# Performance work log

Measured on AMD Instinct MI355X. Metric: run time of the kernel, lower is better.

Reference implementation:

```python
import jax, jax.numpy as jnp
import numpy as np

EMB = 1024
NHEAD = 16
HEAD_DIM = EMB // NHEAD  # 64
L = 2048
NEG = -1e30


def setup_inputs() -> dict:
    key = jax.random.key(0)
    ks = jax.random.split(key, 8)
    # xavier_uniform bound for square [EMB, EMB] matrices
    bound = float(np.sqrt(6.0 / (EMB + EMB)))
    def xavier(k):
        return jax.random.uniform(k, (EMB, EMB), jnp.float32, -bound, bound)
    return {
        "q": jax.random.normal(ks[0], (L, EMB), jnp.float32),
        "k": jax.random.normal(ks[1], (L, EMB), jnp.float32),
        "v": jax.random.normal(ks[2], (L, EMB), jnp.float32),
        "mask": jax.random.randint(ks[3], (NHEAD, L, L), 0, 2) > 0,
        "Wq": xavier(ks[4]),
        "Wk": xavier(ks[5]),
        "Wv": xavier(ks[6]),
        "Wo": xavier(ks[7]),
    }


def reference(q, k, v, mask, Wq, Wk, Wv, Wo):
    scaling = HEAD_DIM ** -0.5
    # F.linear(x, W) = x @ W.T ; reshape to [H, L, D]
    Q = (q @ Wq.T).reshape(L, NHEAD, HEAD_DIM).swapaxes(0, 1)
    K = (k @ Wk.T).reshape(L, NHEAD, HEAD_DIM).swapaxes(0, 1)
    V = (v @ Wv.T).reshape(L, NHEAD, HEAD_DIM).swapaxes(0, 1)
    scores = jnp.einsum("hld,hmd->hlm", Q, K) * scaling  # [H, L, L]
    scores = jnp.where(mask, jnp.asarray(NEG, scores.dtype), scores)
    p = jax.nn.softmax(scores, axis=-1)
    # attn_mask=True: multiplicative re-mask after softmax (custom path)
    p = p * (~mask).astype(p.dtype)
    # dropout is a no-op in eval mode
    attn_out = jnp.einsum("hlm,hmd->hld", p, V)  # [H, L, D]
    attn_out = attn_out.swapaxes(0, 1).reshape(L, EMB)
    return attn_out @ Wo.T
```

## Files before the change

### kernel.cpp

```cpp
#include <hip/hip_runtime.h>
#include <stdint.h>

#define EMB   1024
#define NHEAD 16
#define HDIM  64
#define SEQ   2048

typedef unsigned short ushort_t;
typedef unsigned int   uint32;
typedef __attribute__((ext_vector_type(8))) short bfrag;
typedef __attribute__((ext_vector_type(4))) float ffrag;

#define MFMA(a, b, c) __builtin_amdgcn_mfma_f32_16x16x32_bf16((a), (b), (c), 0, 0, 0)

__device__ inline ushort_t f2bf(float f) {
  uint32 u = __float_as_uint(f);
  u += 0x7FFFu + ((u >> 16) & 1u);
  return (ushort_t)(u >> 16);
}
__device__ inline uint32 pack2(float a, float b) {
  return (uint32)f2bf(a) | ((uint32)f2bf(b) << 16);
}

__device__ inline void glds16(const ushort_t* g, ushort_t* l) {
  __builtin_amdgcn_global_load_lds(
      (const __attribute__((address_space(1))) uint32*)(uintptr_t)g,
      (__attribute__((address_space(3))) uint32*)(uintptr_t)l, 16, 0, 0);
}

__global__ void detect_mask_kernel(const uint32* __restrict__ mw, int* __restrict__ flag) {
  uint32 w = mw[threadIdx.x];
  bool is4 = (w == 0u) || (w == 1u) || (w == 0x3F800000u);
  unsigned long long bad = __ballot(!is4);
  if (threadIdx.x == 0) flag[0] = (bad == 0ull) ? 1 : 0;
}

__global__ __launch_bounds__(256) void compress_mask(
    const void* __restrict__ maskp, const int* __restrict__ flag, ushort_t* __restrict__ bm)
{
  size_t t = (size_t)blockIdx.x * 256 + threadIdx.x;
  size_t row = t >> 7;
  int c16 = (int)(t & 127);
  size_t base = row * SEQ + (size_t)c16 * 16;
  ushort_t mv = 0;
  if (*flag) {
    const uint4* p = (const uint4*)((const uint32*)maskp + base);
    uint4 a0 = p[0], a1 = p[1], a2 = p[2], a3 = p[3];
    uint32 aw[16] = {a0.x,a0.y,a0.z,a0.w, a1.x,a1.y,a1.z,a1.w,
                     a2.x,a2.y,a2.z,a2.w, a3.x,a3.y,a3.z,a3.w};
    #pragma unroll
    for (int i = 0; i < 16; ++i) mv |= (ushort_t)((aw[i] != 0u) ? 1u : 0u) << i;
  } else {
    uint4 b0 = *(const uint4*)((const unsigned char*)maskp + base);
    uint32 bw[4] = {b0.x, b0.y, b0.z, b0.w};
    #pragma unroll
    for (int i = 0; i < 16; ++i)
      mv |= (ushort_t)((((bw[i >> 2] >> ((i & 3) * 8)) & 0xFFu) != 0u) ? 1u : 0u) << i;
  }
  bm[t] = mv;
}

__global__ __launch_bounds__(256) void cvt_all(
    const float4* __restrict__ q,  const float4* __restrict__ k,  const float4* __restrict__ v,
    const float4* __restrict__ wq, const float4* __restrict__ wk, const float4* __restrict__ wv,
    const float4* __restrict__ wo,
    uint2* __restrict__ qb,  uint2* __restrict__ kb,  uint2* __restrict__ vb,
    uint2* __restrict__ wqb, uint2* __restrict__ wkb, uint2* __restrict__ wvb,
    uint2* __restrict__ wob)
{
  int t = blockIdx.x * 256 + threadIdx.x;
  int s = blockIdx.y;
  const float4* src; uint2* dst; int n4;
  switch (s) {
    case 0: src = q;  dst = qb;  n4 = (SEQ * EMB) / 4; break;
    case 1: src = k;  dst = kb;  n4 = (SEQ * EMB) / 4; break;
    case 2: src = v;  dst = vb;  n4 = (SEQ * EMB) / 4; break;
    case 3: src = wq; dst = wqb; n4 = (EMB * EMB) / 4; break;
    case 4: src = wk; dst = wkb; n4 = (EMB * EMB) / 4; break;
    case 5: src = wv; dst = wvb; n4 = (EMB * EMB) / 4; break;
    default: src = wo; dst = wob; n4 = (EMB * EMB) / 4; break;
  }
  if (t >= n4) return;
  float4 f = src[t];
  uint2 o; o.x = pack2(f.x, f.y); o.y = pack2(f.z, f.w);
  dst[t] = o;
}

template<int MODE, int BN>
__device__ inline void gemm_body(const ushort_t* A, const ushort_t* B, void* Cp,
                                 int m0, int n0, ushort_t* As, ushort_t* Bs) {
  const int tid = threadIdx.x, lane = tid & 63, w = tid >> 6;
  const int wm = (w >> 1) * 64, wn = (w & 1) * (BN / 2);
  const int col = lane & 15, g = lane >> 4;
  constexpr int TN = BN / 32;
  constexpr int BIT = BN / 32;

  ffrag acc[4][TN] = {};

  for (int k0 = 0; k0 < EMB; k0 += 64) {
    __syncthreads();
    #pragma unroll
    for (int it = 0; it < 4; ++it) {
      int p = it * 256 + tid;
      int row = p >> 3, pc = p & 7;
      glds16(A + (size_t)(m0 + row) * EMB + k0 + (pc ^ (row & 7)) * 8, &As[p * 8]);
    }
    #pragma unroll
    for (int it = 0; it < BIT; ++it) {
      int p = it * 256 + tid;
      int row = p >> 3, pc = p & 7;
      glds16(B + (size_t)(n0 + row) * EMB + k0 + (pc ^ (row & 7)) * 8, &Bs[p * 8]);
    }
    __syncthreads();

    #pragma unroll
    for (int c = 0; c < 2; ++c) {
      bfrag av[4], bv[TN];
      #pragma unroll
      for (int t = 0; t < 4; ++t) {
        int ra = wm + t * 16 + col;
        av[t] = *(const bfrag*)&As[ra * 64 + ((c * 4 + g) ^ (ra & 7)) * 8];
      }
      #pragma unroll
      for (int t = 0; t < TN; ++t) {
        int rb = wn + t * 16 + col;
        bv[t] = *(const bfrag*)&Bs[rb * 64 + ((c * 4 + g) ^ (rb & 7)) * 8];
      }
      #pragma unroll
      for (int tm = 0; tm < 4; ++tm)
        #pragma unroll
        for (int tn = 0; tn < TN; ++tn)
          acc[tm][tn] = MFMA(av[tm], bv[tn], acc[tm][tn]);
    }
  }

  const int rbase = g * 4;
  #pragma unroll
  for (int tm = 0; tm < 4; ++tm)
    #pragma unroll
    for (int tn = 0; tn < TN; ++tn)
      #pragma unroll
      for (int r = 0; r < 4; ++r) {
        int m = m0 + wm + tm * 16 + rbase + r;
        int n = n0 + wn + tn * 16 + col;
        float vv = acc[tm][tn][r];
        if (MODE == 0) {
          ((ushort_t*)Cp)[((size_t)(n >> 6) * SEQ + m) * HDIM + (n & 63)] = f2bf(vv);
        } else if (MODE == 1) {
          ((ushort_t*)Cp)[((size_t)(m >> 6) * HDIM + (m & 63)) * SEQ + n] = f2bf(vv);
        } else {
          ((float*)Cp)[(size_t)m * EMB + n] = vv;
        }
      }
}

__global__ __launch_bounds__(256) void gemm_qkv(
    const ushort_t* __restrict__ qb, const ushort_t* __restrict__ kb, const ushort_t* __restrict__ vb,
    const ushort_t* __restrict__ Wqb, const ushort_t* __restrict__ Wkb, const ushort_t* __restrict__ Wvb,
    ushort_t* __restrict__ Qb, ushort_t* __restrict__ Kb, ushort_t* __restrict__ Vtb)
{
  __shared__ ushort_t As[128 * 64];
  __shared__ ushort_t Bs[64 * 64];
  const int z = blockIdx.y, bid = blockIdx.x;
  if (z == 0) {
    gemm_body<0, 64>(qb, Wqb, Qb, (bid >> 4) * 128, (bid & 15) * 64, As, Bs);
  } else if (z == 1) {
    gemm_body<0, 64>(kb, Wkb, Kb, (bid >> 4) * 128, (bid & 15) * 64, As, Bs);
  } else {
    gemm_body<1, 64>(Wvb, vb, Vtb, (bid >> 5) * 128, (bid & 31) * 64, As, Bs);
  }
}

__global__ __launch_bounds__(256) void gemm_out(
    const ushort_t* __restrict__ A, const ushort_t* __restrict__ B, float* __restrict__ C)
{
  __shared__ ushort_t As[128 * 64];
  __shared__ ushort_t Bs[64 * 64];
  gemm_body<2, 64>(A, B, (void*)C, blockIdx.y * 128, blockIdx.x * 64, As, Bs);
}

__global__ __launch_bounds__(256) void attn_mfma(
    const ushort_t* __restrict__ Qb,
    const ushort_t* __restrict__ Kb,
    const ushort_t* __restrict__ Vtb,
    const ushort_t* __restrict__ bm,
    ushort_t* __restrict__ attnb)
{
  __shared__ ushort_t KVs[2][2][64 * 64];
  __shared__ ushort_t Ps[4][16 * 72];

  const int tid  = threadIdx.x;
  const int lane = tid & 63;
  const int w    = tid >> 6;
  const int h    = blockIdx.y;
  const int l0   = blockIdx.x * 64;
  const int col  = lane & 15, g = lane >> 4, kg8 = g * 8, rbase = g * 4;

  ushort_t* pw = &Ps[w][0];

  {
    int rl = lane >> 2, seg = (lane & 3) * 16;
    const uint4* pq = (const uint4*)(Qb + ((size_t)h * SEQ + l0 + w * 16 + rl) * HDIM + seg);
    uint4 q0 = pq[0], q1 = pq[1];
    *(uint4*)&pw[rl * 72 + seg] = q0;
    *(uint4*)&pw[rl * 72 + seg + 8] = q1;
  }
  bfrag qf[2];
  qf[0] = *(const bfrag*)&pw[col * 72 + kg8];
  qf[1] = *(const bfrag*)&pw[col * 72 + 32 + kg8];

  auto stage_kv = [&](int kt_, int buf) {
    #pragma unroll
    for (int it = 0; it < 2; ++it) {
      int p = it * 256 + tid;
      int row = p >> 3, pc = p & 7;
      int sc = (pc ^ (row & 7)) * 8;
      glds16(Kb + ((size_t)h * SEQ + kt_ + row) * HDIM + sc, &KVs[buf][0][p * 8]);
      glds16(Vtb + ((size_t)h * HDIM + row) * SEQ + kt_ + sc, &KVs[buf][1][p * 8]);
    }
  };
  stage_kv(0, 0);

  const size_t bmbase = ((size_t)h * SEQ + l0 + w * 16 + (lane >> 2)) * 128 + (lane & 3);
  ushort_t mv_next = bm[bmbase];

  float lsum[4] = {0.f, 0.f, 0.f, 0.f};
  ffrag oacc[4] = {};

  for (int t = 0; t < 32; ++t) {
    const int buf = t & 1;
    __syncthreads();
    stage_kv(((t + 1) & 31) * 64, buf ^ 1);

    const ushort_t* Kc = &KVs[buf][0][0];
    const ushort_t* Vc = &KVs[buf][1][0];

    ushort_t mv = mv_next;
    mv_next = bm[bmbase + ((t + 1) & 31) * 4];

    ffrag s[4] = {};
    #pragma unroll
    for (int c = 0; c < 2; ++c)
      #pragma unroll
      for (int tn = 0; tn < 4; ++tn) {
        int row = tn * 16 + col;
        bfrag kf = *(const bfrag*)&Kc[row * 64 + ((c * 4 + g) ^ (row & 7)) * 8];
        s[tn] = MFMA(qf[c], kf, s[tn]);
      }

    #pragma unroll
    for (int r = 0; r < 4; ++r) {
      #pragma unroll
      for (int tn = 0; tn < 4; ++tn) {
        int m16 = __shfl((int)mv, (rbase + r) * 4 + tn, 64);
        bool msk = ((m16 >> col) & 1) != 0;
        float x = s[tn][r] * 0.125f;
        float p = msk ? 0.f : __expf(x);
        lsum[r] += p;
        pw[(rbase + r) * 72 + tn * 16 + col] = f2bf(p);
      }
    }

    #pragma unroll
    for (int c = 0; c < 2; ++c) {
      bfrag af = *(const bfrag*)&pw[col * 72 + c * 32 + kg8];
      #pragma unroll
      for (int tn = 0; tn < 4; ++tn) {
        int row = tn * 16 + col;
        bfrag vf = *(const bfrag*)&Vc[row * 64 + ((c * 4 + g) ^ (row & 7)) * 8];
        oacc[tn] = MFMA(af, vf, oacc[tn]);
      }
    }
  }

  float inv[4];
  #pragma unroll
  for (int r = 0; r < 4; ++r) {
    float s_ = lsum[r];
    #pragma unroll
    for (int off = 1; off < 16; off <<= 1) s_ += __shfl_xor(s_, off, 64);
    inv[r] = (s_ > 0.f) ? (1.0f / s_) : 0.0f;
  }
  #pragma unroll
  for (int tn = 0; tn < 4; ++tn)
    #pragma unroll
    for (int r = 0; r < 4; ++r) {
      int qg = l0 + w * 16 + rbase + r;
      attnb[(size_t)qg * EMB + h * HDIM + tn * 16 + col] = f2bf(oacc[tn][r] * inv[r]);
    }
}

extern "C" void kernel_launch(void* const* d_in, const int* in_sizes, int n_in,
                              void* d_out, int out_size, void* d_ws, size_t ws_size,
                              hipStream_t stream) {
  const float* q    = (const float*)d_in[0];
  const float* k    = (const float*)d_in[1];
  const float* v    = (const float*)d_in[2];
  const void*  mask =               d_in[3];
  const float* Wq   = (const float*)d_in[4];
  const float* Wk   = (const float*)d_in[5];
  const float* Wv   = (const float*)d_in[6];
  const float* Wo   = (const float*)d_in[7];

  char* ws = (char*)d_ws;
  const size_t MB = 1024 * 1024;
  ushort_t* qb    = (ushort_t*)(ws);
  ushort_t* kb    = (ushort_t*)(ws + 4  * MB);
  ushort_t* vb    = (ushort_t*)(ws + 8  * MB);
  ushort_t* Wqb   = (ushort_t*)(ws + 12 * MB);
  ushort_t* Wkb   = (ushort_t*)(ws + 14 * MB);
  ushort_t* Wvb   = (ushort_t*)(ws + 16 * MB);
  ushort_t* Wob   = (ushort_t*)(ws + 18 * MB);
  ushort_t* Qb    = (ushort_t*)(ws + 20 * MB);
  ushort_t* Kb    = (ushort_t*)(ws + 24 * MB);
  ushort_t* Vtb   = (ushort_t*)(ws + 28 * MB);
  int*      flag  = (int*)     (ws + 32 * MB);
  ushort_t* bmask = (ushort_t*)(ws + 33 * MB);
  ushort_t* attnb = qb;

  detect_mask_kernel<<<1, 64, 0, stream>>>((const uint32*)mask, flag);

  compress_mask<<<16384, 256, 0, stream>>>(mask, flag, bmask);

  cvt_all<<<dim3((SEQ * EMB / 4 + 255) / 256, 7), 256, 0, stream>>>(
      (const float4*)q, (const float4*)k, (const float4*)v,
      (const float4*)Wq, (const float4*)Wk, (const float4*)Wv, (const float4*)Wo,
      (uint2*)qb, (uint2*)kb, (uint2*)vb,
      (uint2*)Wqb, (uint2*)Wkb, (uint2*)Wvb, (uint2*)Wob);

  gemm_qkv<<<dim3(256, 3), 256, 0, stream>>>(qb, kb, vb, Wqb, Wkb, Wvb, Qb, Kb, Vtb);

  attn_mfma<<<dim3(SEQ / 64, NHEAD), 256, 0, stream>>>(Qb, Kb, Vtb, bmask, attnb);

  gemm_out<<<dim3(16, 16), 256, 0, stream>>>(attnb, Wob, (float*)d_out);
}
```

Measured before the change: 482.2 us.

## Merge prep kernels, shrink GEMM tiles, widen attention blocks to 8 waves

Folds mask detection, mask compression and bf16 conversion into one launch, removing two kernel launches. Shrinks the GEMM tiles to 64x64 so the QKV and output projections get twice as many blocks. Widens attention blocks to 512 threads covering 128 query rows, so each staged K/V tile is shared by more waves. The extra redundant mask-format ballot per block is cheap, but the smaller GEMM tiles lower reuse per block, and the larger attention blocks may reduce occupancy.

```diff
diff --git a/kernel.cpp b/kernel.cpp
--- a/kernel.cpp
+++ b/kernel.cpp
@@ -28,117 +28,106 @@
       (__attribute__((address_space(3))) uint32*)(uintptr_t)l, 16, 0, 0);
 }
 
-__global__ void detect_mask_kernel(const uint32* __restrict__ mw, int* __restrict__ flag) {
-  uint32 w = mw[threadIdx.x];
-  bool is4 = (w == 0u) || (w == 1u) || (w == 0x3F800000u);
-  unsigned long long bad = __ballot(!is4);
-  if (threadIdx.x == 0) flag[0] = (bad == 0ull) ? 1 : 0;
-}
-
-__global__ __launch_bounds__(256) void compress_mask(
-    const void* __restrict__ maskp, const int* __restrict__ flag, ushort_t* __restrict__ bm)
-{
-  size_t t = (size_t)blockIdx.x * 256 + threadIdx.x;
-  size_t row = t >> 7;
-  int c16 = (int)(t & 127);
-  size_t base = row * SEQ + (size_t)c16 * 16;
-  ushort_t mv = 0;
-  if (*flag) {
-    const uint4* p = (const uint4*)((const uint32*)maskp + base);
-    uint4 a0 = p[0], a1 = p[1], a2 = p[2], a3 = p[3];
-    uint32 aw[16] = {a0.x,a0.y,a0.z,a0.w, a1.x,a1.y,a1.z,a1.w,
-                     a2.x,a2.y,a2.z,a2.w, a3.x,a3.y,a3.z,a3.w};
-    #pragma unroll
-    for (int i = 0; i < 16; ++i) mv |= (ushort_t)((aw[i] != 0u) ? 1u : 0u) << i;
-  } else {
-    uint4 b0 = *(const uint4*)((const unsigned char*)maskp + base);
-    uint32 bw[4] = {b0.x, b0.y, b0.z, b0.w};
-    #pragma unroll
-    for (int i = 0; i < 16; ++i)
-      mv |= (ushort_t)((((bw[i >> 2] >> ((i & 3) * 8)) & 0xFFu) != 0u) ? 1u : 0u) << i;
-  }
-  bm[t] = mv;
-}
-
-__global__ __launch_bounds__(256) void cvt_all(
+__global__ __launch_bounds__(256) void prep(
     const float4* __restrict__ q,  const float4* __restrict__ k,  const float4* __restrict__ v,
     const float4* __restrict__ wq, const float4* __restrict__ wk, const float4* __restrict__ wv,
-    const float4* __restrict__ wo,
+    const float4* __restrict__ wo, const void* __restrict__ maskp,
     uint2* __restrict__ qb,  uint2* __restrict__ kb,  uint2* __restrict__ vb,
     uint2* __restrict__ wqb, uint2* __restrict__ wkb, uint2* __restrict__ wvb,
-    uint2* __restrict__ wob)
+    uint2* __restrict__ wob, ushort_t* __restrict__ bm)
 {
-  int t = blockIdx.x * 256 + threadIdx.x;
-  int s = blockIdx.y;
-  const float4* src; uint2* dst; int n4;
-  switch (s) {
-    case 0: src = q;  dst = qb;  n4 = (SEQ * EMB) / 4; break;
-    case 1: src = k;  dst = kb;  n4 = (SEQ * EMB) / 4; break;
-    case 2: src = v;  dst = vb;  n4 = (SEQ * EMB) / 4; break;
-    case 3: src = wq; dst = wqb; n4 = (EMB * EMB) / 4; break;
-    case 4: src = wk; dst = wkb; n4 = (EMB * EMB) / 4; break;
-    case 5: src = wv; dst = wvb; n4 = (EMB * EMB) / 4; break;
-    default: src = wo; dst = wob; n4 = (EMB * EMB) / 4; break;
-  }
-  if (t >= n4) return;
-  float4 f = src[t];
-  uint2 o; o.x = pack2(f.x, f.y); o.y = pack2(f.z, f.w);
-  dst[t] = o;
-}
-
-template<int MODE, int BN>
-__device__ inline void gemm_body(const ushort_t* A, const ushort_t* B, void* Cp,
-                                 int m0, int n0, ushort_t* As, ushort_t* Bs) {
+  const int tid = threadIdx.x;
+  const int s = blockIdx.y;
+  if (s < 7) {
+    int t = blockIdx.x * 256 + tid;
+    const float4* src; uint2* dst; int n4;
+    switch (s) {
+      case 0: src = q;  dst = qb;  n4 = (SEQ * EMB) / 4; break;
+      case 1: src = k;  dst = kb;  n4 = (SEQ * EMB) / 4; break;
+      case 2: src = v;  dst = vb;  n4 = (SEQ * EMB) / 4; break;
+      case 3: src = wq; dst = wqb; n4 = (EMB * EMB) / 4; break;
+      case 4: src = wk; dst = wkb; n4 = (EMB * EMB) / 4; break;
+      case 5: src = wv; dst = wvb; n4 = (EMB * EMB) / 4; break;
+      default: src = wo; dst = wob; n4 = (EMB * EMB) / 4; break;
+    }
+    if (t >= n4) return;
+    float4 f = src[t];
+    uint2 o; o.x = pack2(f.x, f.y); o.y = pack2(f.z, f.w);
+    dst[t] = o;
+  } else {
+    uint32 w0 = ((const uint32*)maskp)[tid & 63];
+    bool is4 = (w0 == 0u) || (w0 == 1u) || (w0 == 0x3F800000u);
+    int use32 = (__ballot(!is4) == 0ull) ? 1 : 0;
+    #pragma unroll
+    for (int i = 0; i < 8; ++i) {
+      size_t t = (size_t)i * (2048 * 256) + (size_t)blockIdx.x * 256 + tid;
+      size_t row = t >> 7;
+      int c16 = (int)(t & 127);
+      size_t base = row * SEQ + (size_t)c16 * 16;
+      ushort_t mv = 0;
+      if (use32) {
+        const uint4* p = (const uint4*)((const uint32*)maskp + base);
+        uint4 a0 = p[0], a1 = p[1], a2 = p[2], a3 = p[3];
+        uint32 aw[16] = {a0.x,a0.y,a0.z,a0.w, a1.x,a1.y,a1.z,a1.w,
+                         a2.x,a2.y,a2.z,a2.w, a3.x,a3.y,a3.z,a3.w};
+        #pragma unroll
+        for (int j = 0; j < 16; ++j) mv |= (ushort_t)((aw[j] != 0u) ? 1u : 0u) << j;
+      } else {
+        uint4 b0 = *(const uint4*)((const unsigned char*)maskp + base);
+        uint32 bw[4] = {b0.x, b0.y, b0.z, b0.w};
+        #pragma unroll
+        for (int j = 0; j < 16; ++j)
+          mv |= (ushort_t)((((bw[j >> 2] >> ((j & 3) * 8)) & 0xFFu) != 0u) ? 1u : 0u) << j;
+      }
+      bm[t] = mv;
+    }
+  }
+}
+
+template<int MODE>
+__device__ inline void gemm_body64(const ushort_t* A, const ushort_t* B, void* Cp,
+                                   int m0, int n0, ushort_t* As, ushort_t* Bs) {
   const int tid = threadIdx.x, lane = tid & 63, w = tid >> 6;
-  const int wm = (w >> 1) * 64, wn = (w & 1) * (BN / 2);
+  const int wm = (w >> 1) * 32, wn = (w & 1) * 32;
   const int col = lane & 15, g = lane >> 4;
-  constexpr int TN = BN / 32;
-  constexpr int BIT = BN / 32;
-
-  ffrag acc[4][TN] = {};
+
+  ffrag acc[2][2] = {};
 
   for (int k0 = 0; k0 < EMB; k0 += 64) {
     __syncthreads();
     #pragma unroll
-    for (int it = 0; it < 4; ++it) {
+    for (int it = 0; it < 2; ++it) {
       int p = it * 256 + tid;
       int row = p >> 3, pc = p & 7;
-      glds16(A + (size_t)(m0 + row) * EMB + k0 + (pc ^ (row & 7)) * 8, &As[p * 8]);
-    }
-    #pragma unroll
-    for (int it = 0; it < BIT; ++it) {
-      int p = it * 256 + tid;
-      int row = p >> 3, pc = p & 7;
-      glds16(B + (size_t)(n0 + row) * EMB + k0 + (pc ^ (row & 7)) * 8, &Bs[p * 8]);
+      int sc = (pc ^ (row & 7)) * 8;
+      glds16(A + (size_t)(m0 + row) * EMB + k0 + sc, &As[p * 8]);
+      glds16(B + (size_t)(n0 + row) * EMB + k0 + sc, &Bs[p * 8]);
     }
     __syncthreads();
 
     #pragma unroll
     for (int c = 0; c < 2; ++c) {
-      bfrag av[4], bv[TN];
-      #pragma unroll
-      for (int t = 0; t < 4; ++t) {
+      bfrag av[2], bv[2];
+      #pragma unroll
+      for (int t = 0; t < 2; ++t) {
         int ra = wm + t * 16 + col;
         av[t] = *(const bfrag*)&As[ra * 64 + ((c * 4 + g) ^ (ra & 7)) * 8];
-      }
-      #pragma unroll
-      for (int t = 0; t < TN; ++t) {
         int rb = wn + t * 16 + col;
         bv[t] = *(const bfrag*)&Bs[rb * 64 + ((c * 4 + g) ^ (rb & 7)) * 8];
       }
       #pragma unroll
-      for (int tm = 0; tm < 4; ++tm)
+      for (int tm = 0; tm < 2; ++tm)
         #pragma unroll
-        for (int tn = 0; tn < TN; ++tn)
+        for (int tn = 0; tn < 2; ++tn)
           acc[tm][tn] = MFMA(av[tm], bv[tn], acc[tm][tn]);
     }
   }
 
   const int rbase = g * 4;
   #pragma unroll
-  for (int tm = 0; tm < 4; ++tm)
-    #pragma unroll
-    for (int tn = 0; tn < TN; ++tn)
+  for (int tm = 0; tm < 2; ++tm)
+    #pragma unroll
+    for (int tn = 0; tn < 2; ++tn)
       #pragma unroll
       for (int r = 0; r < 4; ++r) {
         int m = m0 + wm + tm * 16 + rbase + r;
@@ -159,27 +148,27 @@
     const ushort_t* __restrict__ Wqb, const ushort_t* __restrict__ Wkb, const ushort_t* __restrict__ Wvb,
     ushort_t* __restrict__ Qb, ushort_t* __restrict__ Kb, ushort_t* __restrict__ Vtb)
 {
-  __shared__ ushort_t As[128 * 64];
+  __shared__ ushort_t As[64 * 64];
   __shared__ ushort_t Bs[64 * 64];
   const int z = blockIdx.y, bid = blockIdx.x;
   if (z == 0) {
-    gemm_body<0, 64>(qb, Wqb, Qb, (bid >> 4) * 128, (bid & 15) * 64, As, Bs);
+    gemm_body64<0>(qb, Wqb, Qb, (bid >> 4) * 64, (bid & 15) * 64, As, Bs);
   } else if (z == 1) {
-    gemm_body<0, 64>(kb, Wkb, Kb, (bid >> 4) * 128, (bid & 15) * 64, As, Bs);
+    gemm_body64<0>(kb, Wkb, Kb, (bid >> 4) * 64, (bid & 15) * 64, As, Bs);
   } else {
-    gemm_body<1, 64>(Wvb, vb, Vtb, (bid >> 5) * 128, (bid & 31) * 64, As, Bs);
+    gemm_body64<1>(Wvb, vb, Vtb, (bid >> 5) * 64, (bid & 31) * 64, As, Bs);
   }
 }
 
 __global__ __launch_bounds__(256) void gemm_out(
     const ushort_t* __restrict__ A, const ushort_t* __restrict__ B, float* __restrict__ C)
 {
-  __shared__ ushort_t As[128 * 64];
+  __shared__ ushort_t As[64 * 64];
   __shared__ ushort_t Bs[64 * 64];
-  gemm_body<2, 64>(A, B, (void*)C, blockIdx.y * 128, blockIdx.x * 64, As, Bs);
-}
-
-__global__ __launch_bounds__(256) void attn_mfma(
+  gemm_body64<2>(A, B, (void*)C, blockIdx.y * 64, blockIdx.x * 64, As, Bs);
+}
+
+__global__ __launch_bounds__(512, 4) void attn_mfma(
     const ushort_t* __restrict__ Qb,
     const ushort_t* __restrict__ Kb,
     const ushort_t* __restrict__ Vtb,
@@ -187,13 +176,13 @@
     ushort_t* __restrict__ attnb)
 {
   __shared__ ushort_t KVs[2][2][64 * 64];
-  __shared__ ushort_t Ps[4][16 * 72];
+  __shared__ ushort_t Ps[8][16 * 72];
 
   const int tid  = threadIdx.x;
   const int lane = tid & 63;
   const int w    = tid >> 6;
   const int h    = blockIdx.y;
-  const int l0   = blockIdx.x * 64;
+  const int l0   = blockIdx.x * 128;
   const int col  = lane & 15, g = lane >> 4, kg8 = g * 8, rbase = g * 4;
 
   ushort_t* pw = &Ps[w][0];
@@ -210,14 +199,11 @@
   qf[1] = *(const bfrag*)&pw[col * 72 + 32 + kg8];
 
   auto stage_kv = [&](int kt_, int buf) {
-    #pragma unroll
-    for (int it = 0; it < 2; ++it) {
-      int p = it * 256 + tid;
-      int row = p >> 3, pc = p & 7;
-      int sc = (pc ^ (row & 7)) * 8;
-      glds16(Kb + ((size_t)h * SEQ + kt_ + row) * HDIM + sc, &KVs[buf][0][p * 8]);
-      glds16(Vtb + ((size_t)h * HDIM + row) * SEQ + kt_ + sc, &KVs[buf][1][p * 8]);
-    }
+    int p = tid;
+    int row = p >> 3, pc = p & 7;
+    int sc = (pc ^ (row & 7)) * 8;
+    glds16(Kb + ((size_t)h * SEQ + kt_ + row) * HDIM + sc, &KVs[buf][0][p * 8]);
+    glds16(Vtb + ((size_t)h * HDIM + row) * SEQ + kt_ + sc, &KVs[buf][1][p * 8]);
   };
   stage_kv(0, 0);
 
@@ -314,23 +300,18 @@
   ushort_t* Qb    = (ushort_t*)(ws + 20 * MB);
   ushort_t* Kb    = (ushort_t*)(ws + 24 * MB);
   ushort_t* Vtb   = (ushort_t*)(ws + 28 * MB);
-  int*      flag  = (int*)     (ws + 32 * MB);
   ushort_t* bmask = (ushort_t*)(ws + 33 * MB);
   ushort_t* attnb = qb;
 
-  detect_mask_kernel<<<1, 64, 0, stream>>>((const uint32*)mask, flag);
-
-  compress_mask<<<16384, 256, 0, stream>>>(mask, flag, bmask);
-
-  cvt_all<<<dim3((SEQ * EMB / 4 + 255) / 256, 7), 256, 0, stream>>>(
+  prep<<<dim3(2048, 8), 256, 0, stream>>>(
       (const float4*)q, (const float4*)k, (const float4*)v,
-      (const float4*)Wq, (const float4*)Wk, (const float4*)Wv, (const float4*)Wo,
+      (const float4*)Wq, (const float4*)Wk, (const float4*)Wv, (const float4*)Wo, mask,
       (uint2*)qb, (uint2*)kb, (uint2*)vb,
-      (uint2*)Wqb, (uint2*)Wkb, (uint2*)Wvb, (uint2*)Wob);
-
-  gemm_qkv<<<dim3(256, 3), 256, 0, stream>>>(qb, kb, vb, Wqb, Wkb, Wvb, Qb, Kb, Vtb);
-
-  attn_mfma<<<dim3(SEQ / 64, NHEAD), 256, 0, stream>>>(Qb, Kb, Vtb, bmask, attnb);
-
-  gemm_out<<<dim3(16, 16), 256, 0, stream>>>(attnb, Wob, (float*)d_out);
-}
+      (uint2*)Wqb, (uint2*)Wkb, (uint2*)Wvb, (uint2*)Wob, bmask);
+
+  gemm_qkv<<<dim3(512, 3), 256, 0, stream>>>(qb, kb, vb, Wqb, Wkb, Wvb, Qb, Kb, Vtb);
+
+  attn_mfma<<<dim3(SEQ / 128, NHEAD), 512, 0, stream>>>(Qb, Kb, Vtb, bmask, attnb);
+
+  gemm_out<<<dim3(16, 32), 256, 0, stream>>>(attnb, Wob, (float*)d_out);
+}
```

Result: no change. 489.7 us (+1.5%).
